# Kernel tuning notes

Measured on AMD Instinct MI355X. Metric: run time of the kernel, lower is better.

## Reference

```python
import jax, jax.numpy as jnp
import numpy as np

INPUT_SIZE = 1024
HIDDEN_SIZE = 1024
LN_EPS = 1e-5


def setup_inputs() -> dict:
    key = jax.random.key(0)
    ks = jax.random.split(key, 8)
    bs, n = 4, 2048
    # Xavier-uniform bound for square (in=out) linear layers
    bound = float(np.sqrt(6.0 / (INPUT_SIZE + HIDDEN_SIZE)))
    x = jax.random.normal(ks[0], (bs, n, INPUT_SIZE), dtype=jnp.float32)
    wq = jax.random.uniform(ks[1], (INPUT_SIZE, HIDDEN_SIZE), jnp.float32, -bound, bound)
    wk = jax.random.uniform(ks[2], (INPUT_SIZE, HIDDEN_SIZE), jnp.float32, -bound, bound)
    wv = jax.random.uniform(ks[3], (INPUT_SIZE, HIDDEN_SIZE), jnp.float32, -bound, bound)
    bq = jnp.zeros((HIDDEN_SIZE,), jnp.float32)
    bk = jnp.zeros((HIDDEN_SIZE,), jnp.float32)
    bv = jnp.zeros((HIDDEN_SIZE,), jnp.float32)
    ln_w = jnp.ones((INPUT_SIZE,), jnp.float32)
    ln_b = jnp.zeros((INPUT_SIZE,), jnp.float32)
    return {"x": x, "wq": wq, "bq": bq, "wk": wk, "bk": bk,
            "wv": wv, "bv": bv, "ln_w": ln_w, "ln_b": ln_b}


def _layernorm(x, w, b):
    mu = jnp.mean(x, axis=-1, keepdims=True)
    var = jnp.mean(jnp.square(x - mu), axis=-1, keepdims=True)
    return (x - mu) * jax.lax.rsqrt(var + LN_EPS) * w + b


def reference(x, wq, bq, wk, bk, wv, bv, ln_w, ln_b):
    # x: [b, n, d_in]
    xn = _layernorm(x, ln_w, ln_b)
    q = jnp.einsum('bnd,dh->bnh', xn, wq) + bq
    k = jnp.einsum('bnd,dh->bnh', xn, wk) + bk
    v = jnp.einsum('bnd,dh->bnh', xn, wv) + bv
    scale = 1.0 / np.sqrt(HIDDEN_SIZE)
    att = jnp.einsum('bqh,bkh->bqk', q, k) * scale  # [b, n, n]
    att = jax.nn.softmax(att, axis=-1)
    out = jnp.einsum('bqk,bkh->bqh', att, v)  # [b, n, h]
    return (att, out)
```

## Files before the change

### kernel.cpp

```cpp
#include <hip/hip_runtime.h>
#include <stdint.h>


typedef __attribute__((ext_vector_type(8))) short short8;
typedef __attribute__((ext_vector_type(4))) float floatx4;
typedef __attribute__((ext_vector_type(4))) uint16_t u16x4;

__device__ __forceinline__ uint16_t f2bf(float f) {
    union { float f; uint32_t u; } v; v.f = f;
    uint32_t r = v.u + 0x7fffu + ((v.u >> 16) & 1u);
    return (uint16_t)(r >> 16);
}

typedef const uint32_t __attribute__((address_space(1)))* gas1_t;
typedef uint32_t __attribute__((address_space(3)))* las3_t;
__device__ __forceinline__ void gload_lds16(const uint16_t* g, uint16_t* l) {
    __builtin_amdgcn_global_load_lds((gas1_t)g, (las3_t)l, 16, 0, 0);
}

#define BM 128
#define BN 128
#define BK2 64

template<int EPI>
__device__ __forceinline__ void gemm_bt_body(
    const uint16_t* __restrict__ A, const uint16_t* __restrict__ Bt, int K,
    float* __restrict__ Cf, uint16_t* __restrict__ Cb, int ldc,
    const float* __restrict__ bias, float alpha)
{
    __shared__ uint16_t lA[BM * BK2];
    __shared__ uint16_t lB[BN * BK2];

    const int t  = threadIdx.x;
    const int m0 = blockIdx.y * BM;
    const int n0 = blockIdx.x * BN;

    const int srow = t >> 3;
    const int sseg = (t & 7) ^ (srow & 7);
    const uint16_t* ga = A + (size_t)(m0 + srow) * K + sseg * 8;
    const uint16_t* gb = Bt + (size_t)(n0 + srow) * K + sseg * 8;
    uint16_t* la = &lA[t * 8];
    uint16_t* lb = &lB[t * 8];
    const size_t rstep = (size_t)32 * K;

    const int lane = t & 63;
    const int w    = t >> 6;
    const int quad = lane >> 4;
    const int lrow = lane & 15;
    const int wm   = (w & 1) * 64;
    const int wn   = (w >> 1) * 64;
    const int swz  = lrow & 7;

    floatx4 acc[4][4];
#pragma unroll
    for (int i = 0; i < 4; i++)
#pragma unroll
        for (int j = 0; j < 4; j++)
            acc[i][j] = floatx4{0.f, 0.f, 0.f, 0.f};

    for (int k0 = 0; k0 < K; k0 += BK2) {
        __syncthreads();
        gload_lds16(ga + k0,             la);
        gload_lds16(ga + rstep + k0,     la + 2048);
        gload_lds16(ga + 2 * rstep + k0, la + 4096);
        gload_lds16(ga + 3 * rstep + k0, la + 6144);
        gload_lds16(gb + k0,             lb);
        gload_lds16(gb + rstep + k0,     lb + 2048);
        gload_lds16(gb + 2 * rstep + k0, lb + 4096);
        gload_lds16(gb + 3 * rstep + k0, lb + 6144);
        __syncthreads();

#pragma unroll
        for (int ks = 0; ks < 2; ks++) {
            short8 af[4], bf[4];
#pragma unroll
            for (int mi = 0; mi < 4; mi++)
                af[mi] = *(const short8*)&lA[(wm + mi * 16 + lrow) * BK2 +
                                             (((ks * 4 + quad) ^ swz) * 8)];
#pragma unroll
            for (int ni = 0; ni < 4; ni++)
                bf[ni] = *(const short8*)&lB[(wn + ni * 16 + lrow) * BK2 +
                                             (((ks * 4 + quad) ^ swz) * 8)];
#pragma unroll
            for (int mi = 0; mi < 4; mi++)
#pragma unroll
                for (int ni = 0; ni < 4; ni++)
                    acc[mi][ni] = __builtin_amdgcn_mfma_f32_16x16x32_bf16(
                        af[mi], bf[ni], acc[mi][ni], 0, 0, 0);
        }
    }

#pragma unroll
    for (int mi = 0; mi < 4; mi++) {
#pragma unroll
        for (int ni = 0; ni < 4; ni++) {
            const int row = m0 + wm + mi * 16 + quad * 4;
            const int col = n0 + wn + ni * 16 + lrow;
#pragma unroll
            for (int r = 0; r < 4; r++) {
                const float v = acc[mi][ni][r];
                if (EPI == 0) {
                    Cf[(size_t)(row + r) * ldc + col] = v * alpha;
                } else if (EPI == 1) {
                    Cb[(size_t)(row + r) * ldc + col] = f2bf(v + bias[col]);
                } else {
                    Cf[(size_t)(row + r) * ldc + col] = v;
                }
            }
        }
    }
}

__global__ __launch_bounds__(256) void k_qkv(
    const uint16_t* __restrict__ xn, const uint16_t* __restrict__ wt,
    const float* __restrict__ bq, const float* __restrict__ bk,
    const float* __restrict__ bv, uint16_t* __restrict__ qkv)
{
    const int z = blockIdx.z;
    const uint16_t* Bt = wt + (size_t)z * 1024 * 1024;
    const float* bias = (z == 0) ? bq : ((z == 1) ? bk : bv);
    uint16_t* C = qkv + (size_t)z * 8192 * 1024;
    gemm_bt_body<1>(xn, Bt, 1024, nullptr, C, 1024, bias, 0.f);
}

__global__ __launch_bounds__(256) void k_scores(
    const uint16_t* __restrict__ q, const uint16_t* __restrict__ k,
    float* __restrict__ S)
{
    const int z = blockIdx.z;
    gemm_bt_body<0>(q + (size_t)z * 2048 * 1024, k + (size_t)z * 2048 * 1024, 1024,
                    S + (size_t)z * 2048 * 2048, nullptr, 2048, nullptr, 0.03125f);
}

__global__ __launch_bounds__(256) void k_out(
    const uint16_t* __restrict__ attb, const uint16_t* __restrict__ vt,
    float* __restrict__ out)
{
    const int z = blockIdx.z;
    gemm_bt_body<2>(attb + (size_t)z * 2048 * 2048, vt + (size_t)z * 1024 * 2048, 2048,
                    out + (size_t)z * 2048 * 1024, nullptr, 1024, nullptr, 0.f);
}

__global__ __launch_bounds__(256) void k_ln(
    const float* __restrict__ x, const float* __restrict__ lw,
    const float* __restrict__ lb, uint16_t* __restrict__ xn)
{
    const int row = blockIdx.x;
    const int t = threadIdx.x;
    const float* xr = x + (size_t)row * 1024;
    const float4 xv = ((const float4*)xr)[t];
    float s  = xv.x + xv.y + xv.z + xv.w;
    float s2 = xv.x * xv.x + xv.y * xv.y + xv.z * xv.z + xv.w * xv.w;
#pragma unroll
    for (int off = 32; off > 0; off >>= 1) {
        s  += __shfl_xor(s, off);
        s2 += __shfl_xor(s2, off);
    }
    __shared__ float ps[4], ps2[4];
    const int w = t >> 6, lane = t & 63;
    if (lane == 0) { ps[w] = s; ps2[w] = s2; }
    __syncthreads();
    s  = ps[0] + ps[1] + ps[2] + ps[3];
    s2 = ps2[0] + ps2[1] + ps2[2] + ps2[3];
    const float mu  = s * (1.f / 1024.f);
    const float var = s2 * (1.f / 1024.f) - mu * mu;
    const float rs  = rsqrtf(var + 1e-5f);
    const float4 wv = ((const float4*)lw)[t];
    const float4 bv = ((const float4*)lb)[t];
    u16x4 o;
    o.x = f2bf((xv.x - mu) * rs * wv.x + bv.x);
    o.y = f2bf((xv.y - mu) * rs * wv.y + bv.y);
    o.z = f2bf((xv.z - mu) * rs * wv.z + bv.z);
    o.w = f2bf((xv.w - mu) * rs * wv.w + bv.w);
    ((u16x4*)(xn + (size_t)row * 1024))[t] = o;
}

__global__ void k_wt(const float* __restrict__ wq, const float* __restrict__ wk,
                     const float* __restrict__ wv, uint16_t* __restrict__ wt)
{
    __shared__ float tile[32][33];
    const int z = blockIdx.z;
    const float* W = (z == 0) ? wq : ((z == 1) ? wk : wv);
    uint16_t* T = wt + (size_t)z * 1024 * 1024;
    const int c0 = blockIdx.x * 32, r0 = blockIdx.y * 32;
    const int tx = threadIdx.x, ty = threadIdx.y;
#pragma unroll
    for (int i = 0; i < 4; i++)
        tile[ty + 8 * i][tx] = W[(size_t)(r0 + ty + 8 * i) * 1024 + c0 + tx];
    __syncthreads();
#pragma unroll
    for (int i = 0; i < 4; i++)
        T[(size_t)(c0 + ty + 8 * i) * 1024 + r0 + tx] = f2bf(tile[tx][ty + 8 * i]);
}

__global__ __launch_bounds__(256) void k_vt(
    const uint16_t* __restrict__ v, uint16_t* __restrict__ vt)
{
    __shared__ uint16_t tile[64][68];
    const int b = blockIdx.z;
    const uint16_t* V = v + (size_t)b * 2048 * 1024;
    uint16_t* T = vt + (size_t)b * 1024 * 2048;
    const int h0 = blockIdx.x * 64, t0 = blockIdx.y * 64;
    const int t = threadIdx.x;
    const int rr = t >> 4;
    const int cc = (t & 15) * 4;
#pragma unroll
    for (int i = 0; i < 4; i++) {
        const int tok = rr + 16 * i;
        *(u16x4*)&tile[tok][cc] =
            *(const u16x4*)&V[(size_t)(t0 + tok) * 1024 + h0 + cc];
    }
    __syncthreads();
#pragma unroll
    for (int i = 0; i < 4; i++) {
        const int h = rr + 16 * i;
        u16x4 o;
        o.x = tile[cc + 0][h];
        o.y = tile[cc + 1][h];
        o.z = tile[cc + 2][h];
        o.w = tile[cc + 3][h];
        *(u16x4*)&T[(size_t)(h0 + h) * 2048 + t0 + cc] = o;
    }
}

__global__ __launch_bounds__(256) void k_softmax(
    float* __restrict__ S, uint16_t* __restrict__ attb)
{
    const size_t row = blockIdx.x;
    float* p = S + row * 2048;
    const int t = threadIdx.x;
    float4 a = ((float4*)p)[2 * t];
    float4 b = ((float4*)p)[2 * t + 1];
    float m = fmaxf(fmaxf(fmaxf(a.x, a.y), fmaxf(a.z, a.w)),
                    fmaxf(fmaxf(b.x, b.y), fmaxf(b.z, b.w)));
#pragma unroll
    for (int off = 32; off > 0; off >>= 1) m = fmaxf(m, __shfl_xor(m, off));
    __shared__ float pm[4], pl[4];
    const int w = t >> 6, lane = t & 63;
    if (lane == 0) pm[w] = m;
    __syncthreads();
    m = fmaxf(fmaxf(pm[0], pm[1]), fmaxf(pm[2], pm[3]));

    a.x = __expf(a.x - m); a.y = __expf(a.y - m);
    a.z = __expf(a.z - m); a.w = __expf(a.w - m);
    b.x = __expf(b.x - m); b.y = __expf(b.y - m);
    b.z = __expf(b.z - m); b.w = __expf(b.w - m);
    float s = a.x + a.y + a.z + a.w + b.x + b.y + b.z + b.w;
#pragma unroll
    for (int off = 32; off > 0; off >>= 1) s += __shfl_xor(s, off);
    if (lane == 0) pl[w] = s;
    __syncthreads();
    s = pl[0] + pl[1] + pl[2] + pl[3];
    const float inv = 1.f / s;

    a.x *= inv; a.y *= inv; a.z *= inv; a.w *= inv;
    b.x *= inv; b.y *= inv; b.z *= inv; b.w *= inv;
    ((float4*)p)[2 * t]     = a;
    ((float4*)p)[2 * t + 1] = b;

    uint16_t* q = attb + row * 2048 + t * 8;
    u16x4 o0, o1;
    o0.x = f2bf(a.x); o0.y = f2bf(a.y); o0.z = f2bf(a.z); o0.w = f2bf(a.w);
    o1.x = f2bf(b.x); o1.y = f2bf(b.y); o1.z = f2bf(b.z); o1.w = f2bf(b.w);
    ((u16x4*)q)[0] = o0;
    ((u16x4*)q)[1] = o1;
}

extern "C" void kernel_launch(void* const* d_in, const int* in_sizes, int n_in,
                              void* d_out, int out_size, void* d_ws, size_t ws_size,
                              hipStream_t stream)
{
    const float* x  = (const float*)d_in[0];
    const float* wq = (const float*)d_in[1];
    const float* bq = (const float*)d_in[2];
    const float* wk = (const float*)d_in[3];
    const float* bk = (const float*)d_in[4];
    const float* wv = (const float*)d_in[5];
    const float* bv = (const float*)d_in[6];
    const float* lw = (const float*)d_in[7];
    const float* lb = (const float*)d_in[8];

    float* att = (float*)d_out;
    float* out = (float*)d_out + (size_t)16777216;

    uint16_t* xn = (uint16_t*)d_out;
    uint16_t* wt = (uint16_t*)d_out + (size_t)8388608;

    uint16_t* ws   = (uint16_t*)d_ws;
    uint16_t* q    = ws;
    uint16_t* k    = ws + (size_t)8388608;
    uint16_t* v    = ws + (size_t)2 * 8388608;
    uint16_t* vt   = ws;
    uint16_t* attb = ws + (size_t)8388608;
    uint16_t* qkv  = q;

    if (ws_size < (size_t)50331648) return;

    k_ln<<<8192, 256, 0, stream>>>(x, lw, lb, xn);
    k_wt<<<dim3(32, 32, 3), dim3(32, 8), 0, stream>>>(wq, wk, wv, wt);
    k_qkv<<<dim3(8, 64, 3), 256, 0, stream>>>(xn, wt, bq, bk, bv, qkv);
    k_scores<<<dim3(16, 16, 4), 256, 0, stream>>>(q, k, att);
    k_vt<<<dim3(16, 32, 4), 256, 0, stream>>>(v, vt);
    k_softmax<<<8192, 256, 0, stream>>>(att, attb);
    k_out<<<dim3(8, 16, 4), 256, 0, stream>>>(attb, vt, out);
}
```

Measured before the change: 337.4 us.

## Use 256x256 pipelined GEMM tiles for QKV projection and attention scores

Replaces the 128x128 GEMM body for the QKV projection and score kernels with a 512-thread 256x256 tile kernel. It double-buffers LDS via direct global-to-LDS loads, uses XOR-swizzled LDS reads, interleaves staging with MFMA quarters under explicit barriers and setprio, and remaps block IDs so neighbouring blocks share data in cache. The QKV GEMM is merged into one N=3072 launch over concatenated weights. Larger tiles raise data reuse and cut LDS/global traffic, but use 128KB of LDS and many registers, which limits occupancy; the hand-written waitcnt schedule is fragile.

```diff
diff --git a/kernel.cpp b/kernel.cpp
--- a/kernel.cpp
+++ b/kernel.cpp
@@ -16,6 +16,213 @@
 typedef uint32_t __attribute__((address_space(3)))* las3_t;
 __device__ __forceinline__ void gload_lds16(const uint16_t* g, uint16_t* l) {
     __builtin_amdgcn_global_load_lds((gas1_t)g, (las3_t)l, 16, 0, 0);
+}
+
+__device__ __forceinline__ void s_bar()  { asm volatile("s_barrier" ::: "memory"); }
+__device__ __forceinline__ void lgkm0()  { asm volatile("s_waitcnt lgkmcnt(0)" ::: "memory"); }
+template<int N> __device__ __forceinline__ void vmw() {
+    asm volatile("s_waitcnt vmcnt(%0)" :: "n"(N) : "memory");
+}
+
+template<int EPI>
+__device__ __forceinline__ void gemm256(
+    const uint16_t* __restrict__ A, const uint16_t* __restrict__ Bt,
+    const int K, const int NT, const int m0, const int n0,
+    float* __restrict__ Cf, uint16_t* __restrict__ Cb, const int ldc,
+    const float* __restrict__ bq, const float* __restrict__ bk,
+    const float* __restrict__ bv, const float alpha)
+{
+    __shared__ uint16_t sm[65536];
+
+    const int t = threadIdx.x;
+
+    const int srow = t >> 3;
+    const int sseg = (t & 7) ^ (srow & 7);
+    const uint16_t* gA = A + (size_t)(m0 + srow) * K + sseg * 8;
+    const uint16_t* gB = Bt + (size_t)(n0 + srow) * K + sseg * 8;
+    uint16_t* ldst = sm + t * 8;
+
+    auto STAGE = [&](int kt, int h) {
+        kt = (kt < NT) ? kt : (NT - 2);
+        const uint16_t* g = (h & 2) ? gB : gA;
+        const size_t roff = (size_t)(h & 1) * 128 * K + (size_t)kt * 64;
+        uint16_t* d = ldst + (kt & 1) * 32768 + (h & 2) * 8192 + (h & 1) * 8192;
+        gload_lds16(g + roff, d);
+        gload_lds16(g + roff + (size_t)64 * K, d + 4096);
+    };
+
+    const int lane = t & 63;
+    const int wid  = t >> 6;
+    const int wm   = wid >> 2;
+    const int wn   = wid & 3;
+    const int quad = lane >> 4;
+    const int lrow = lane & 15;
+    const int swz  = lrow & 7;
+    const int ksg0 = (quad ^ swz) * 8;
+    const int ksg1 = ((4 + quad) ^ swz) * 8;
+    const int aoff = (wm * 128 + lrow) * 64;
+    const int boff = (wn * 64 + lrow) * 64;
+
+    const uint16_t* lA0 = sm;
+    const uint16_t* lB0 = sm + 16384;
+    const uint16_t* lA1 = sm + 32768;
+    const uint16_t* lB1 = sm + 49152;
+
+#define RDA(P, mi, ks) (*(const short8*)((P) + aoff + (mi) * 1024 + ((ks) ? ksg1 : ksg0)))
+#define RDB(P, ni, ks) (*(const short8*)((P) + boff + (ni) * 1024 + ((ks) ? ksg1 : ksg0)))
+
+    floatx4 acc[8][4];
+#pragma unroll
+    for (int mi = 0; mi < 8; ++mi)
+#pragma unroll
+        for (int ni = 0; ni < 4; ++ni)
+            acc[mi][ni] = floatx4{0.f, 0.f, 0.f, 0.f};
+
+    short8 Af[8][2], Bf[4][2];
+
+#define READ_A(P, MI0)                                   \
+    _Pragma("unroll")                                    \
+    for (int mi = 0; mi < 4; ++mi) {                     \
+        Af[MI0 + mi][0] = RDA(P, MI0 + mi, 0);           \
+        Af[MI0 + mi][1] = RDA(P, MI0 + mi, 1);           \
+    }
+#define READ_B(P, NI0)                                   \
+    _Pragma("unroll")                                    \
+    for (int ni = 0; ni < 2; ++ni) {                     \
+        Bf[NI0 + ni][0] = RDB(P, NI0 + ni, 0);           \
+        Bf[NI0 + ni][1] = RDB(P, NI0 + ni, 1);           \
+    }
+#define MFMA_Q(MI0, NI0)                                                     \
+    __builtin_amdgcn_s_setprio(1);                                           \
+    _Pragma("unroll")                                                        \
+    for (int mi = MI0; mi < MI0 + 4; ++mi)                                   \
+        _Pragma("unroll")                                                    \
+        for (int ni = NI0; ni < NI0 + 2; ++ni)                               \
+            _Pragma("unroll")                                                \
+            for (int ks = 0; ks < 2; ++ks)                                   \
+                acc[mi][ni] = __builtin_amdgcn_mfma_f32_16x16x32_bf16(       \
+                    Af[mi][ks], Bf[ni][ks], acc[mi][ni], 0, 0, 0);           \
+    __builtin_amdgcn_s_setprio(0);
+
+    STAGE(0, 0); STAGE(0, 1); STAGE(0, 2); STAGE(0, 3);
+    STAGE(1, 0); STAGE(1, 1);
+    vmw<4>();
+    s_bar();
+
+    const int NI = NT >> 1;
+    for (int it = 0; it < NI; ++it) {
+        const int te = it * 2;
+
+        READ_A(lA0, 0); READ_B(lB0, 0);
+        STAGE(te + 1, 2);
+        s_bar(); lgkm0();
+        MFMA_Q(0, 0);
+        s_bar();
+        READ_A(lA0, 4); READ_B(lB0, 2);
+        STAGE(te + 1, 3);
+        s_bar(); lgkm0();
+        MFMA_Q(4, 2);
+        s_bar();
+        STAGE(te + 2, 0);
+        s_bar();
+        MFMA_Q(0, 2);
+        s_bar();
+        STAGE(te + 2, 1);
+        s_bar();
+        MFMA_Q(4, 0);
+        vmw<4>();
+        s_bar();
+
+        READ_A(lA1, 0); READ_B(lB1, 0);
+        STAGE(te + 2, 2);
+        s_bar(); lgkm0();
+        MFMA_Q(0, 0);
+        s_bar();
+        READ_A(lA1, 4); READ_B(lB1, 2);
+        STAGE(te + 2, 3);
+        s_bar(); lgkm0();
+        MFMA_Q(4, 2);
+        s_bar();
+        STAGE(te + 3, 0);
+        s_bar();
+        MFMA_Q(0, 2);
+        s_bar();
+        STAGE(te + 3, 1);
+        s_bar();
+        MFMA_Q(4, 0);
+        vmw<4>();
+        s_bar();
+    }
+
+    vmw<0>();
+
+    const int rbase = m0 + wm * 128 + quad * 4;
+    const int cbase = n0 + wn * 64 + lrow;
+
+    if (EPI == 1) {
+        float bc[4];
+        const float* bias[3] = {bq, bk, bv};
+#pragma unroll
+        for (int ni = 0; ni < 4; ++ni) {
+            const int col = cbase + ni * 16;
+            bc[ni] = bias[col >> 10][col & 1023];
+        }
+#pragma unroll
+        for (int mi = 0; mi < 8; ++mi) {
+#pragma unroll
+            for (int ni = 0; ni < 4; ++ni) {
+                const int row = rbase + mi * 16;
+                const int col = cbase + ni * 16;
+                const int z = col >> 10, h = col & 1023;
+#pragma unroll
+                for (int r = 0; r < 4; ++r)
+                    Cb[(size_t)z * 8388608 + (size_t)(row + r) * 1024 + h] =
+                        f2bf(acc[mi][ni][r] + bc[ni]);
+            }
+        }
+    } else {
+#pragma unroll
+        for (int mi = 0; mi < 8; ++mi) {
+#pragma unroll
+            for (int ni = 0; ni < 4; ++ni) {
+                const int row = rbase + mi * 16;
+                const int col = cbase + ni * 16;
+#pragma unroll
+                for (int r = 0; r < 4; ++r)
+                    Cf[(size_t)(row + r) * ldc + col] = acc[mi][ni][r] * alpha;
+            }
+        }
+    }
+#undef RDA
+#undef RDB
+#undef READ_A
+#undef READ_B
+#undef MFMA_Q
+}
+
+__global__ __launch_bounds__(512, 2) void k_qkv(
+    const uint16_t* __restrict__ xn, const uint16_t* __restrict__ wt,
+    const float* __restrict__ bq, const float* __restrict__ bk,
+    const float* __restrict__ bv, uint16_t* __restrict__ qkv)
+{
+    const int flat = blockIdx.y * 12 + blockIdx.x;
+    const int s = (flat & 7) * 48 + (flat >> 3);
+    const int bx = s % 12, by = s / 12;
+    gemm256<1>(xn, wt, 1024, 16, by * 256, bx * 256,
+               nullptr, qkv, 0, bq, bk, bv, 0.f);
+}
+
+__global__ __launch_bounds__(512, 2) void k_scores(
+    const uint16_t* __restrict__ q, const uint16_t* __restrict__ k,
+    float* __restrict__ S)
+{
+    const int flat = blockIdx.z * 64 + blockIdx.y * 8 + blockIdx.x;
+    const int s = (flat & 7) * 32 + (flat >> 3);
+    const int z = s >> 6, y = (s >> 3) & 7, x = s & 7;
+    gemm256<0>(q + (size_t)z * 2048 * 1024, k + (size_t)z * 2048 * 1024,
+               1024, 16, y * 256, x * 256,
+               S + (size_t)z * 2048 * 2048, nullptr, 2048,
+               nullptr, nullptr, nullptr, 0.03125f);
 }
 
 #define BM 128
@@ -109,27 +316,6 @@
             }
         }
     }
-}
-
-__global__ __launch_bounds__(256) void k_qkv(
-    const uint16_t* __restrict__ xn, const uint16_t* __restrict__ wt,
-    const float* __restrict__ bq, const float* __restrict__ bk,
-    const float* __restrict__ bv, uint16_t* __restrict__ qkv)
-{
-    const int z = blockIdx.z;
-    const uint16_t* Bt = wt + (size_t)z * 1024 * 1024;
-    const float* bias = (z == 0) ? bq : ((z == 1) ? bk : bv);
-    uint16_t* C = qkv + (size_t)z * 8192 * 1024;
-    gemm_bt_body<1>(xn, Bt, 1024, nullptr, C, 1024, bias, 0.f);
-}
-
-__global__ __launch_bounds__(256) void k_scores(
-    const uint16_t* __restrict__ q, const uint16_t* __restrict__ k,
-    float* __restrict__ S)
-{
-    const int z = blockIdx.z;
-    gemm_bt_body<0>(q + (size_t)z * 2048 * 1024, k + (size_t)z * 2048 * 1024, 1024,
-                    S + (size_t)z * 2048 * 2048, nullptr, 2048, nullptr, 0.03125f);
 }
 
 __global__ __launch_bounds__(256) void k_out(
@@ -298,8 +484,8 @@
 
     k_ln<<<8192, 256, 0, stream>>>(x, lw, lb, xn);
     k_wt<<<dim3(32, 32, 3), dim3(32, 8), 0, stream>>>(wq, wk, wv, wt);
-    k_qkv<<<dim3(8, 64, 3), 256, 0, stream>>>(xn, wt, bq, bk, bv, qkv);
-    k_scores<<<dim3(16, 16, 4), 256, 0, stream>>>(q, k, att);
+    k_qkv<<<dim3(12, 32), 512, 0, stream>>>(xn, wt, bq, bk, bv, qkv);
+    k_scores<<<dim3(8, 8, 4), 512, 0, stream>>>(q, k, att);
     k_vt<<<dim3(16, 32, 4), 256, 0, stream>>>(v, vt);
     k_softmax<<<8192, 256, 0, stream>>>(att, attb);
     k_out<<<dim3(8, 16, 4), 256, 0, stream>>>(attb, vt, out);
```

Measured after the change: 323.5 us. 1.04x faster.

## Rewrite GEMMs as 512-thread large-tile multi-buffered pipelines with XCD-aware block swizzle

Applied to the files above, without the earlier changes.

Replaces the simple 128x128 single-buffered GEMM body with a 256xBN tile kernel using 8 waves, double/triple LDS buffering with async global->LDS prefetch two stages ahead, interleaved LDS reads and MFMA clusters with setprio, and raw barriers/waitcnts. The QKV projection is fused into one wide N=3072 GEMM with 192-wide tiles, and block indices are remapped so consecutive blocks land on different XCDs. It targets the load-compute serialization and low arithmetic intensity of the old kernel, at the cost of higher register/LDS use and fragile hand-written synchronization.

```diff
diff --git a/kernel.cpp b/kernel.cpp
--- a/kernel.cpp
+++ b/kernel.cpp
@@ -18,127 +18,236 @@
     __builtin_amdgcn_global_load_lds((gas1_t)g, (las3_t)l, 16, 0, 0);
 }
 
-#define BM 128
-#define BN 128
-#define BK2 64
-
-template<int EPI>
-__device__ __forceinline__ void gemm_bt_body(
-    const uint16_t* __restrict__ A, const uint16_t* __restrict__ Bt, int K,
-    float* __restrict__ Cf, uint16_t* __restrict__ Cb, int ldc,
-    const float* __restrict__ bias, float alpha)
-{
-    __shared__ uint16_t lA[BM * BK2];
-    __shared__ uint16_t lB[BN * BK2];
-
-    const int t  = threadIdx.x;
-    const int m0 = blockIdx.y * BM;
-    const int n0 = blockIdx.x * BN;
+__device__ __forceinline__ void s_bar()  { asm volatile("s_barrier" ::: "memory"); }
+__device__ __forceinline__ void lgkm0()  { asm volatile("s_waitcnt lgkmcnt(0)" ::: "memory"); }
+template<int N> __device__ __forceinline__ void vmw() {
+    asm volatile("s_waitcnt vmcnt(%0)" :: "n"(N) : "memory");
+}
+
+
+#define RA(MF, MI)                                                        \
+    { Af[(MF)][0] = *(const short8*)(LA + aoff + (MI) * 1024 + ksg0);     \
+      Af[(MF)][1] = *(const short8*)(LA + aoff + (MI) * 1024 + ksg1); }
+#define RB(NI)                                                            \
+    { Bf[(NI)][0] = *(const short8*)(LB + boff + (NI) * 1024 + ksg0);     \
+      Bf[(NI)][1] = *(const short8*)(LB + boff + (NI) * 1024 + ksg1); }
+#define CLUST(MA, MF, NI0)                                                \
+    __builtin_amdgcn_s_setprio(1);                                        \
+    _Pragma("unroll") for (int mi = 0; mi < 4; ++mi)                      \
+    _Pragma("unroll") for (int nn = 0; nn < 2; ++nn)                      \
+    _Pragma("unroll") for (int ks = 0; ks < 2; ++ks)                      \
+        acc[(MA) + mi][(NI0) + nn] =                                      \
+            __builtin_amdgcn_mfma_f32_16x16x32_bf16(                      \
+                Af[(MF) + mi][ks], Bf[(NI0) + nn][ks],                    \
+                acc[(MA) + mi][(NI0) + nn], 0, 0, 0);                     \
+    __builtin_amdgcn_s_setprio(0);
+#define CLUST1(NI)                                                        \
+    __builtin_amdgcn_s_setprio(1);                                        \
+    _Pragma("unroll") for (int mi = 0; mi < 8; ++mi)                      \
+    _Pragma("unroll") for (int ks = 0; ks < 2; ++ks)                      \
+        acc[mi][(NI)] = __builtin_amdgcn_mfma_f32_16x16x32_bf16(          \
+            Af[mi][ks], Bf[(NI)][ks], acc[mi][(NI)], 0, 0, 0);            \
+    __builtin_amdgcn_s_setprio(0);
+
+template<int BN, int EPI>
+__device__ __forceinline__ void gemm8p(
+    const uint16_t* __restrict__ A, const uint16_t* __restrict__ Bt,
+    const int K, const int NT, const int m0, const int n0,
+    float* __restrict__ Cf, uint16_t* __restrict__ Cb, const int ldc,
+    const float* __restrict__ bq, const float* __restrict__ bk,
+    const float* __restrict__ bv, const float alpha)
+{
+    constexpr int ABUF  = 256 * 64;
+    constexpr int BP    = BN / 64;
+    constexpr int BBUF  = BN * 64;
+    constexpr int BUFSZ = ABUF + BBUF;
+    constexpr int NIW   = BN / 64;
+    constexpr int OPS   = 4 + BP;
+    constexpr int NBUF  = (BN == 128) ? 3 : 2;
+    __shared__ uint16_t sm[NBUF * BUFSZ + 4096];
+    uint16_t* const trash = sm + NBUF * BUFSZ;
+
+    const int t = threadIdx.x;
 
     const int srow = t >> 3;
     const int sseg = (t & 7) ^ (srow & 7);
-    const uint16_t* ga = A + (size_t)(m0 + srow) * K + sseg * 8;
-    const uint16_t* gb = Bt + (size_t)(n0 + srow) * K + sseg * 8;
-    uint16_t* la = &lA[t * 8];
-    uint16_t* lb = &lB[t * 8];
-    const size_t rstep = (size_t)32 * K;
+    const uint16_t* gA = A + (size_t)(m0 + srow) * K + sseg * 8;
+    const uint16_t* gB = Bt + (size_t)(n0 + srow) * K + sseg * 8;
+
+    auto STGALL = [&](int kt, int bi) {
+        const int live = kt < NT;
+        const size_t ko = (size_t)(live ? kt : 0) * 64;
+        uint16_t* const db = sm + bi * BUFSZ + t * 8;
+        uint16_t* const tr = trash + t * 8;
+#pragma unroll
+        for (int p = 0; p < 4; ++p)
+            gload_lds16(gA + (size_t)(p * 64) * K + ko,
+                        live ? (db + p * 4096) : tr);
+#pragma unroll
+        for (int p = 0; p < BP; ++p)
+            gload_lds16(gB + (size_t)(p * 64) * K + ko,
+                        live ? (db + ABUF + p * 4096) : tr);
+    };
 
     const int lane = t & 63;
-    const int w    = t >> 6;
+    const int wid  = t >> 6;
+    const int wm   = wid >> 2;
+    const int wn   = wid & 3;
     const int quad = lane >> 4;
     const int lrow = lane & 15;
-    const int wm   = (w & 1) * 64;
-    const int wn   = (w >> 1) * 64;
     const int swz  = lrow & 7;
-
-    floatx4 acc[4][4];
-#pragma unroll
-    for (int i = 0; i < 4; i++)
-#pragma unroll
-        for (int j = 0; j < 4; j++)
-            acc[i][j] = floatx4{0.f, 0.f, 0.f, 0.f};
-
-    for (int k0 = 0; k0 < K; k0 += BK2) {
-        __syncthreads();
-        gload_lds16(ga + k0,             la);
-        gload_lds16(ga + rstep + k0,     la + 2048);
-        gload_lds16(ga + 2 * rstep + k0, la + 4096);
-        gload_lds16(ga + 3 * rstep + k0, la + 6144);
-        gload_lds16(gb + k0,             lb);
-        gload_lds16(gb + rstep + k0,     lb + 2048);
-        gload_lds16(gb + 2 * rstep + k0, lb + 4096);
-        gload_lds16(gb + 3 * rstep + k0, lb + 6144);
-        __syncthreads();
-
-#pragma unroll
-        for (int ks = 0; ks < 2; ks++) {
-            short8 af[4], bf[4];
-#pragma unroll
-            for (int mi = 0; mi < 4; mi++)
-                af[mi] = *(const short8*)&lA[(wm + mi * 16 + lrow) * BK2 +
-                                             (((ks * 4 + quad) ^ swz) * 8)];
-#pragma unroll
-            for (int ni = 0; ni < 4; ni++)
-                bf[ni] = *(const short8*)&lB[(wn + ni * 16 + lrow) * BK2 +
-                                             (((ks * 4 + quad) ^ swz) * 8)];
-#pragma unroll
-            for (int mi = 0; mi < 4; mi++)
-#pragma unroll
-                for (int ni = 0; ni < 4; ni++)
-                    acc[mi][ni] = __builtin_amdgcn_mfma_f32_16x16x32_bf16(
-                        af[mi], bf[ni], acc[mi][ni], 0, 0, 0);
+    const int ksg0 = (quad ^ swz) * 8;
+    const int ksg1 = ((4 + quad) ^ swz) * 8;
+    const int aoff = (wm * 128 + lrow) * 64;
+    const int boff = (wn * (16 * NIW) + lrow) * 64;
+
+    floatx4 acc[8][NIW];
+#pragma unroll
+    for (int mi = 0; mi < 8; ++mi)
+#pragma unroll
+        for (int ni = 0; ni < NIW; ++ni)
+            acc[mi][ni] = floatx4{0.f, 0.f, 0.f, 0.f};
+
+    short8 Af[(BN == 192) ? 8 : 4][2];
+    short8 Bf[NIW][2];
+
+    STGALL(0, 0);
+    STGALL(1, 1);
+    vmw<OPS>();
+    s_bar();
+
+    int bcur = 0, bstage = 2;
+    for (int te = 0; te < NT; ++te) {
+        const int bi = (BN == 128) ? bcur : (te & 1);
+        const uint16_t* LA = sm + bi * BUFSZ;
+        const uint16_t* LB = LA + ABUF;
+
+        if constexpr (BN == 256) {
+            RA(0, 0) RA(1, 1) RA(2, 2) RA(3, 3) RB(0) RB(1)
+            s_bar(); lgkm0();
+            CLUST(0, 0, 0)
+            s_bar();
+            RB(2) RB(3)
+            s_bar(); lgkm0();
+            CLUST(0, 0, 2)
+            s_bar();
+            RA(0, 4) RA(1, 5) RA(2, 6) RA(3, 7)
+            s_bar(); lgkm0();
+            CLUST(4, 0, 0)
+            s_bar();
+            STGALL(te + 2, bi);
+            s_bar();
+            CLUST(4, 0, 2)
+            vmw<OPS>();
+            s_bar();
+        } else if constexpr (BN == 192) {
+            RA(0, 0) RA(1, 1) RA(2, 2) RA(3, 3) RB(0) RB(1)
+            s_bar(); lgkm0();
+            CLUST(0, 0, 0)
+            s_bar();
+            RA(4, 4) RA(5, 5) RA(6, 6) RA(7, 7) RB(2)
+            s_bar(); lgkm0();
+            CLUST(4, 4, 0)
+            s_bar();
+            STGALL(te + 2, bi);
+            s_bar();
+            CLUST1(2)
+            vmw<OPS>();
+            s_bar();
+        } else {
+            STGALL(te + 2, bstage);
+            RA(0, 0) RA(1, 1) RA(2, 2) RA(3, 3) RB(0) RB(1)
+            s_bar(); lgkm0();
+            CLUST(0, 0, 0)
+            s_bar();
+            RA(0, 4) RA(1, 5) RA(2, 6) RA(3, 7)
+            s_bar(); lgkm0();
+            CLUST(4, 0, 0)
+            vmw<OPS>();
+            s_bar();
+            bcur   = (bcur == 2) ? 0 : bcur + 1;
+            bstage = (bstage == 2) ? 0 : bstage + 1;
         }
     }
 
-#pragma unroll
-    for (int mi = 0; mi < 4; mi++) {
-#pragma unroll
-        for (int ni = 0; ni < 4; ni++) {
-            const int row = m0 + wm + mi * 16 + quad * 4;
-            const int col = n0 + wn + ni * 16 + lrow;
-#pragma unroll
-            for (int r = 0; r < 4; r++) {
-                const float v = acc[mi][ni][r];
-                if (EPI == 0) {
-                    Cf[(size_t)(row + r) * ldc + col] = v * alpha;
-                } else if (EPI == 1) {
-                    Cb[(size_t)(row + r) * ldc + col] = f2bf(v + bias[col]);
-                } else {
-                    Cf[(size_t)(row + r) * ldc + col] = v;
-                }
+    vmw<0>();
+
+    const int rbase = m0 + wm * 128 + quad * 4;
+    const int cbase = n0 + wn * (16 * NIW) + lrow;
+
+    if constexpr (EPI == 1) {
+        float bc[NIW];
+#pragma unroll
+        for (int ni = 0; ni < NIW; ++ni) {
+            const int col = cbase + ni * 16;
+            const int z = col >> 10;
+            const float* bp = (z == 0) ? bq : ((z == 1) ? bk : bv);
+            bc[ni] = bp[col & 1023];
+        }
+#pragma unroll
+        for (int mi = 0; mi < 8; ++mi) {
+#pragma unroll
+            for (int ni = 0; ni < NIW; ++ni) {
+                const int row = rbase + mi * 16;
+                const int col = cbase + ni * 16;
+                const int z = col >> 10, h = col & 1023;
+#pragma unroll
+                for (int r = 0; r < 4; ++r)
+                    Cb[(size_t)z * 8388608 + (size_t)(row + r) * 1024 + h] =
+                        f2bf(acc[mi][ni][r] + bc[ni]);
+            }
+        }
+    } else {
+#pragma unroll
+        for (int mi = 0; mi < 8; ++mi) {
+#pragma unroll
+            for (int ni = 0; ni < NIW; ++ni) {
+                const int row = rbase + mi * 16;
+                const int col = cbase + ni * 16;
+#pragma unroll
+                for (int r = 0; r < 4; ++r)
+                    Cf[(size_t)(row + r) * ldc + col] = acc[mi][ni][r] * alpha;
             }
         }
     }
 }
 
-__global__ __launch_bounds__(256) void k_qkv(
+__global__ __launch_bounds__(512, 2) void k_qkv(
     const uint16_t* __restrict__ xn, const uint16_t* __restrict__ wt,
     const float* __restrict__ bq, const float* __restrict__ bk,
     const float* __restrict__ bv, uint16_t* __restrict__ qkv)
 {
-    const int z = blockIdx.z;
-    const uint16_t* Bt = wt + (size_t)z * 1024 * 1024;
-    const float* bias = (z == 0) ? bq : ((z == 1) ? bk : bv);
-    uint16_t* C = qkv + (size_t)z * 8192 * 1024;
-    gemm_bt_body<1>(xn, Bt, 1024, nullptr, C, 1024, bias, 0.f);
-}
-
-__global__ __launch_bounds__(256) void k_scores(
+    const int flat = blockIdx.y * 16 + blockIdx.x;
+    const int s = (flat & 7) * 64 + (flat >> 3);
+    const int bx = s & 15, by = s >> 4;
+    gemm8p<192, 1>(xn, wt, 1024, 16, by * 256, bx * 192,
+                   nullptr, qkv, 0, bq, bk, bv, 0.f);
+}
+
+__global__ __launch_bounds__(512, 2) void k_scores(
     const uint16_t* __restrict__ q, const uint16_t* __restrict__ k,
     float* __restrict__ S)
 {
-    const int z = blockIdx.z;
-    gemm_bt_body<0>(q + (size_t)z * 2048 * 1024, k + (size_t)z * 2048 * 1024, 1024,
-                    S + (size_t)z * 2048 * 2048, nullptr, 2048, nullptr, 0.03125f);
-}
-
-__global__ __launch_bounds__(256) void k_out(
+    const int flat = blockIdx.z * 64 + blockIdx.y * 8 + blockIdx.x;
+    const int s = (flat & 7) * 32 + (flat >> 3);
+    const int z = s >> 6, y = (s >> 3) & 7, x = s & 7;
+    gemm8p<256, 0>(q + (size_t)z * 2048 * 1024, k + (size_t)z * 2048 * 1024,
+                   1024, 16, y * 256, x * 256,
+                   S + (size_t)z * 2048 * 2048, nullptr, 2048,
+                   nullptr, nullptr, nullptr, 0.03125f);
+}
+
+__global__ __launch_bounds__(512, 2) void k_out(
     const uint16_t* __restrict__ attb, const uint16_t* __restrict__ vt,
     float* __restrict__ out)
 {
-    const int z = blockIdx.z;
-    gemm_bt_body<2>(attb + (size_t)z * 2048 * 2048, vt + (size_t)z * 1024 * 2048, 2048,
-                    out + (size_t)z * 2048 * 1024, nullptr, 1024, nullptr, 0.f);
+    const int flat = blockIdx.z * 64 + blockIdx.y * 8 + blockIdx.x;
+    const int s = (flat & 7) * 32 + (flat >> 3);
+    const int z = s >> 6, y = (s >> 3) & 7, x = s & 7;
+    gemm8p<128, 0>(attb + (size_t)z * 2048 * 2048, vt + (size_t)z * 1024 * 2048,
+                   2048, 32, y * 256, x * 128,
+                   out + (size_t)z * 2048 * 1024, nullptr, 1024,
+                   nullptr, nullptr, nullptr, 1.0f);
 }
 
 __global__ __launch_bounds__(256) void k_ln(
@@ -298,9 +407,9 @@
 
     k_ln<<<8192, 256, 0, stream>>>(x, lw, lb, xn);
     k_wt<<<dim3(32, 32, 3), dim3(32, 8), 0, stream>>>(wq, wk, wv, wt);
-    k_qkv<<<dim3(8, 64, 3), 256, 0, stream>>>(xn, wt, bq, bk, bv, qkv);
-    k_scores<<<dim3(16, 16, 4), 256, 0, stream>>>(q, k, att);
+    k_qkv<<<dim3(16, 32), 512, 0, stream>>>(xn, wt, bq, bk, bv, qkv);
+    k_scores<<<dim3(8, 8, 4), 512, 0, stream>>>(q, k, att);
     k_vt<<<dim3(16, 32, 4), 256, 0, stream>>>(v, vt);
     k_softmax<<<8192, 256, 0, stream>>>(att, attb);
-    k_out<<<dim3(8, 16, 4), 256, 0, stream>>>(attb, vt, out);
-}
+    k_out<<<dim3(8, 8, 4), 512, 0, stream>>>(attb, vt, out);
+}
```

Measured after the change: 314.7 us. 1.07x faster.
